# Optimization experiments

Hardware: AMD Instinct MI355X
Metric: run time of the kernel (lower is better)

The kernel has to match this reference:

```python
import jax, jax.numpy as jnp
import numpy as np

N, D0, D1, D2 = 8192, 512, 256, 64


def setup_inputs() -> dict:
    key = jax.random.key(0)
    k1, k2, k3, k4 = jax.random.split(key, 4)
    xi = jax.random.normal(k1, (N, D0), dtype=jnp.float32)
    # graph filter ~ row-normalized adjacency: nonnegative, entries O(1/N)
    filter_matrix = jax.random.uniform(k2, (N, N), dtype=jnp.float32) * (2.0 / N)
    b1 = np.sqrt(6.0 / (D0 + D1))
    b2 = np.sqrt(6.0 / (D1 + D2))
    w1 = jax.random.uniform(k3, (D0, D1), dtype=jnp.float32, minval=-b1, maxval=b1)
    w2 = jax.random.uniform(k4, (D1, D2), dtype=jnp.float32, minval=-b2, maxval=b2)
    return {"xi": xi, "filter_matrix": filter_matrix, "w1": w1, "w2": w2}


def reference(xi, filter_matrix, w1, w2):
    # two GCN layers: F @ (X @ W)
    h = jax.nn.relu(filter_matrix @ (xi @ w1))          # [N, D1]
    emb = filter_matrix @ (h @ w2)                       # [N, D2]
    # pairwise squared Euclidean distances between rows of emb -> [N, N]
    sq = jnp.sum(emb * emb, axis=1)                      # [N]
    dists = jnp.maximum(sq[:, None] + sq[None, :] - 2.0 * (emb @ emb.T), 0.0)
    recons_w = jax.nn.softmax(-dists, axis=1)            # row softmax of negative distances
    return emb, recons_w + 1e-10
```

## Files before the change

### kernel.cpp

```cpp
#include <hip/hip_runtime.h>

typedef short s16x8 __attribute__((ext_vector_type(8)));
typedef float f32x4 __attribute__((ext_vector_type(4)));
typedef unsigned int u32;

#define DEV static __device__ __forceinline__

DEV unsigned short f2bf(float x){
  u32 u = __builtin_bit_cast(u32, x);
  return (unsigned short)((u + 0x7FFFu + ((u >> 16) & 1u)) >> 16);
}
DEV float bf2f(unsigned short h){ u32 u = ((u32)h) << 16; return __builtin_bit_cast(float, u); }
DEV u32 pack2(float a, float b){ return (u32)f2bf(a) | ((u32)f2bf(b) << 16); }

DEV void gld16(const void* g, void* l){
  __builtin_amdgcn_global_load_lds((const __attribute__((address_space(1))) u32*)g,
                                   (__attribute__((address_space(3))) u32*)l, 16, 0, 0);
}

template<int N> DEV void vmwait(){
  static_assert(N>=0 && N<=8, "vmcnt range");
  if constexpr (N==0) asm volatile("s_waitcnt vmcnt(0)" ::: "memory");
  else if constexpr (N==1) asm volatile("s_waitcnt vmcnt(1)" ::: "memory");
  else if constexpr (N==2) asm volatile("s_waitcnt vmcnt(2)" ::: "memory");
  else if constexpr (N==3) asm volatile("s_waitcnt vmcnt(3)" ::: "memory");
  else if constexpr (N==4) asm volatile("s_waitcnt vmcnt(4)" ::: "memory");
  else if constexpr (N==5) asm volatile("s_waitcnt vmcnt(5)" ::: "memory");
  else if constexpr (N==6) asm volatile("s_waitcnt vmcnt(6)" ::: "memory");
  else if constexpr (N==7) asm volatile("s_waitcnt vmcnt(7)" ::: "memory");
  else                     asm volatile("s_waitcnt vmcnt(8)" ::: "memory");
}
DEV void pipebar(){
  __builtin_amdgcn_sched_barrier(0);
  __builtin_amdgcn_s_barrier();
  __builtin_amdgcn_sched_barrier(0);
}

__global__ void k_cvt(const float* __restrict__ src, unsigned short* __restrict__ dst, long n4){
  long i = (long)blockIdx.x*256 + threadIdx.x;
  long stride = (long)gridDim.x*256;
  for (; i < n4; i += stride){
    float4 v = ((const float4*)src)[i];
    int2 p; p.x = (int)pack2(v.x, v.y); p.y = (int)pack2(v.z, v.w);
    ((int2*)dst)[i] = p;
  }
}

__global__ void k_transpose_bf16(const float* __restrict__ src,
                                 unsigned short* __restrict__ dst, int R, int C){
  int idx = blockIdx.x * 256 + threadIdx.x;
  if (idx >= R * C) return;
  int r = idx / C, c = idx % C;
  dst[(size_t)c * R + r] = f2bf(src[idx]);
}

__global__ void k_relu_bf16(const float* __restrict__ src, unsigned short* __restrict__ dst, int n4){
  int idx = blockIdx.x*256 + threadIdx.x;
  if (idx >= n4) return;
  float4 v = ((const float4*)src)[idx];
  int2 p;
  p.x = (int)pack2(fmaxf(v.x,0.f), fmaxf(v.y,0.f));
  p.y = (int)pack2(fmaxf(v.z,0.f), fmaxf(v.w,0.f));
  ((int2*)dst)[idx] = p;
}

template<int ROWS,int BK,int THREADS>
DEV void stage_lds(const unsigned short* __restrict__ src, int row0, int ld,
                   int kk, char* lds, int tid){
  constexpr int SLOTS = BK/8, SLM = SLOTS-1, RPC = 64/SLOTS;
  constexpr int NCH = ROWS*BK*2/1024;
  constexpr int NW = THREADS/64, NI = NCH/NW;
  static_assert(NI*NW==NCH, "chunk exact");
  const int lane = tid & 63, wid = tid >> 6;
  #pragma unroll
  for (int i=0;i<NI;i++){
    int c = i*NW + wid;
    int r = c*RPC + lane/SLOTS;
    int s = lane & SLM;
    int ks = s ^ (r & SLM);
    gld16(src + (size_t)(row0+r)*ld + kk + ks*8, lds + c*1024);
  }
}

template<int BM,int BN,int BK,int WR,int WC,bool ATOMIC>
__global__ __launch_bounds__(WR*WC*64)
void k_gemm(const unsigned short* __restrict__ A, const unsigned short* __restrict__ B,
            void* __restrict__ Cp, int lda, int ldb, int ldc, int kchunk)
{
  constexpr int THREADS = WR*WC*64;
  constexpr int ROWB = BK*2, SLM = BK/8 - 1;
  constexpr int TBYTES = (BM+BN)*ROWB;
  constexpr int WM = BM/WR, WN = BN/WC;
  constexpr int FM = WM/16, FN = WN/16, KS = BK/32;
  constexpr int LA = BM*BK*2/1024/(THREADS/64);
  constexpr int LB = BN*BK*2/1024/(THREADS/64);
  constexpr int L  = LA + LB;

  __shared__ char smem[3*TBYTES];

  const int tid = threadIdx.x, lane = tid & 63;
  const int wid = tid >> 6, wrr = wid / WC, wcc = wid % WC;
  const int m0 = blockIdx.y * BM, n0 = blockIdx.x * BN;
  const int kbeg = blockIdx.z * kchunk, nk = kchunk / BK;

  f32x4 acc[FM][FN];
  f32x4 z4 = {0.f,0.f,0.f,0.f};
  #pragma unroll
  for (int m=0;m<FM;m++)
    #pragma unroll
    for (int n=0;n<FN;n++) acc[m][n] = z4;

  auto stage = [&](int kk, char* b){
    stage_lds<BM,BK,THREADS>(A, m0, lda, kk, b, tid);
    stage_lds<BN,BK,THREADS>(B, n0, ldb, kk, b + BM*ROWB, tid);
  };
  auto compute = [&](const char* b){
    const char* bA = b;
    const char* bB = b + BM*ROWB;
    #pragma unroll
    for (int ks=0;ks<KS;ks++){
      s16x8 av[FM], bv[FN];
      #pragma unroll
      for (int m=0;m<FM;m++){
        int r = wrr*WM + m*16 + (lane&15);
        int s = (ks*4 + (lane>>4)) ^ (r & SLM);
        av[m] = *(const s16x8*)(bA + r*ROWB + s*16);
      }
      #pragma unroll
      for (int n=0;n<FN;n++){
        int r = wcc*WN + n*16 + (lane&15);
        int s = (ks*4 + (lane>>4)) ^ (r & SLM);
        bv[n] = *(const s16x8*)(bB + r*ROWB + s*16);
      }
      #pragma unroll
      for (int m=0;m<FM;m++)
        #pragma unroll
        for (int n=0;n<FN;n++)
          acc[m][n] = __builtin_amdgcn_mfma_f32_16x16x32_bf16(av[m], bv[n], acc[m][n], 0, 0, 0);
    }
  };

  char* bc = smem;
  char* b1 = smem + TBYTES;
  char* b2 = smem + 2*TBYTES;

  stage(kbeg, bc);
  stage(kbeg + BK, b1);

  for (int t=0; t<nk; t++){
    if (t+1 < nk) vmwait<L>();
    else          vmwait<0>();
    pipebar();
    if (t+2 < nk) stage(kbeg + (t+2)*BK, b2);
    compute(bc);
    pipebar();
    char* tmp = bc; bc = b1; b1 = b2; b2 = tmp;
  }

  if constexpr (ATOMIC) {
    float* Cf = (float*)Cp;
    #pragma unroll
    for (int m=0;m<FM;m++)
      #pragma unroll
      for (int n=0;n<FN;n++)
        #pragma unroll
        for (int r=0;r<4;r++){
          int row = m0 + wrr*WM + m*16 + (lane>>4)*4 + r;
          int col = n0 + wcc*WN + n*16 + (lane&15);
          atomicAdd(Cf + (size_t)row*ldc + col, acc[m][n][r]);
        }
  } else {
    unsigned short* Ch = (unsigned short*)Cp;
    #pragma unroll
    for (int m=0;m<FM;m++)
      #pragma unroll
      for (int n=0;n<FN;n++)
        #pragma unroll
        for (int r=0;r<4;r++){
          int row = m0 + wrr*WM + m*16 + (lane>>4)*4 + r;
          int col = n0 + wcc*WN + n*16 + (lane&15);
          Ch[(size_t)row*ldc + col] = f2bf(acc[m][n][r]);
        }
  }
}

__global__ void k_emb_fin(const float* __restrict__ acc, float* __restrict__ emb_out,
                          unsigned short* __restrict__ embb, float* __restrict__ sq){
  int idx = blockIdx.x*256 + threadIdx.x;
  float v = acc[idx];
  emb_out[idx] = v;
  unsigned short ub = f2bf(v);
  embb[idx] = ub;
  float x = bf2f(ub);
  float s = x*x;
  #pragma unroll
  for (int off=32; off>0; off>>=1) s += __shfl_xor(s, off, 64);
  if ((threadIdx.x & 63)==0) sq[idx>>6] = s;
}

template<int PASS>
__global__ __launch_bounds__(256)
void k_dist(const unsigned short* __restrict__ embb, const float* __restrict__ sq,
            float* __restrict__ S, float* __restrict__ out)
{
  constexpr int ROWB = 128, SLM = 7;
  __shared__ char smem[2*128*128];
  char* bufA = smem;
  char* bufB = smem + 128*ROWB;
  const int tid=threadIdx.x, lane=tid&63, wid=tid>>6;
  const int wrr = wid>>1, wcc = wid&1;
  const int i0 = blockIdx.y*128, j0 = blockIdx.x*128;

  #pragma unroll
  for (int i=0;i<4;i++){
    int u = tid + i*256;
    int r = u>>3, c = u&7;
    int byte = r*ROWB + ((c^(r&SLM))*16);
    *(int4*)(bufA+byte) = *(const int4*)(embb + (size_t)(i0+r)*64 + c*8);
    *(int4*)(bufB+byte) = *(const int4*)(embb + (size_t)(j0+r)*64 + c*8);
  }
  __syncthreads();

  f32x4 acc[4][4];
  f32x4 z4 = {0.f,0.f,0.f,0.f};
  #pragma unroll
  for (int m=0;m<4;m++)
    #pragma unroll
    for (int n=0;n<4;n++) acc[m][n]=z4;

  #pragma unroll
  for (int ks=0;ks<2;ks++){
    s16x8 av[4], bv[4];
    #pragma unroll
    for (int m=0;m<4;m++){
      int r = wrr*64 + m*16 + (lane&15);
      int slot = (ks*4 + (lane>>4)) ^ (r&SLM);
      av[m] = *(const s16x8*)(bufA + r*ROWB + slot*16);
    }
    #pragma unroll
    for (int n=0;n<4;n++){
      int r = wcc*64 + n*16 + (lane&15);
      int slot = (ks*4 + (lane>>4)) ^ (r&SLM);
      bv[n] = *(const s16x8*)(bufB + r*ROWB + slot*16);
    }
    #pragma unroll
    for (int m=0;m<4;m++)
      #pragma unroll
      for (int n=0;n<4;n++)
        acc[m][n] = __builtin_amdgcn_mfma_f32_16x16x32_bf16(av[m], bv[n], acc[m][n], 0, 0, 0);
  }

  float sqj[4];
  #pragma unroll
  for (int n=0;n<4;n++) sqj[n] = sq[j0 + wcc*64 + n*16 + (lane&15)];

  #pragma unroll
  for (int m=0;m<4;m++){
    #pragma unroll
    for (int r=0;r<4;r++){
      int row = i0 + wrr*64 + m*16 + (lane>>4)*4 + r;
      float sqi = sq[row];
      if constexpr (PASS==1){
        float v = 0.f;
        #pragma unroll
        for (int n=0;n<4;n++){
          float d = fmaxf(sqi + sqj[n] - 2.f*acc[m][n][r], 0.f);
          v += __expf(-d);
        }
        #pragma unroll
        for (int off=1; off<16; off<<=1) v += __shfl_xor(v, off, 64);
        if ((lane&15)==0) atomicAdd(S+row, v);
      } else {
        float inv = 1.0f / S[row];
        #pragma unroll
        for (int n=0;n<4;n++){
          int col = j0 + wcc*64 + n*16 + (lane&15);
          float d = fmaxf(sqi + sqj[n] - 2.f*acc[m][n][r], 0.f);
          out[(size_t)row*8192 + col] = __expf(-d)*inv + 1e-10f;
        }
      }
    }
  }
}

extern "C" void kernel_launch(void* const* d_in, const int* in_sizes, int n_in,
                              void* d_out, int out_size, void* d_ws, size_t ws_size,
                              hipStream_t stream)
{
  const float* xi = (const float*)d_in[0];
  const float* F  = (const float*)d_in[1];
  const float* w1 = (const float*)d_in[2];
  const float* w2 = (const float*)d_in[3];
  float* out = (float*)d_out;
  float* emb_out = out;
  float* recons  = out + (size_t)8192*64;

  unsigned short* Fb = (unsigned short*)recons;

  char* ws = (char*)d_ws;
  size_t off = 0;
  auto alloc = [&](size_t bytes)->char*{ char* p = ws + off; off += (bytes + 255) & ~(size_t)255; return p; };
  unsigned short* w1t  = (unsigned short*)alloc((size_t)256*512*2);
  unsigned short* w2t  = (unsigned short*)alloc((size_t)64*256*2);
  unsigned short* xib  = (unsigned short*)alloc((size_t)8192*512*2);
  unsigned short* t1t  = (unsigned short*)alloc((size_t)256*8192*2);
  unsigned short* t2t  = (unsigned short*)alloc((size_t)64*8192*2);
  unsigned short* h    = (unsigned short*)alloc((size_t)8192*256*2);
  unsigned short* embb = (unsigned short*)alloc((size_t)8192*64*2);
  float* sq    = (float*)alloc((size_t)8192*4);
  char* zbase = ws + off;
  float* h_acc   = (float*)alloc((size_t)8192*256*4);
  float* emb_acc = (float*)alloc((size_t)8192*64*4);
  float* S       = (float*)alloc((size_t)8192*4);
  size_t zbytes = (size_t)((ws + off) - zbase);

  hipMemsetAsync(zbase, 0, zbytes, stream);

  k_cvt<<<dim3(2048),256,0,stream>>>(F,  Fb,  (long)8192*8192/4);
  k_cvt<<<dim3(2048),256,0,stream>>>(xi, xib, (long)8192*512/4);
  k_transpose_bf16<<<dim3((512*256+255)/256), 256, 0, stream>>>(w1, w1t, 512, 256);
  k_transpose_bf16<<<dim3((256*64+255)/256),  256, 0, stream>>>(w2, w2t, 256, 64);

  k_gemm<128,64,64,2,2,false><<<dim3(128,2,1),256,0,stream>>>(
      w1t, xib, t1t, 512, 512, 8192, 512);

  k_gemm<128,256,32,2,4,true><<<dim3(1,64,8),512,0,stream>>>(
      Fb, t1t, h_acc, 8192, 8192, 256, 1024);

  k_relu_bf16<<<dim3(8192*256/4/256),256,0,stream>>>(h_acc, h, 8192*256/4);

  k_gemm<64,64,64,2,2,false><<<dim3(128,1,1),256,0,stream>>>(
      w2t, h, t2t, 256, 256, 8192, 256);

  k_gemm<128,64,64,2,2,true><<<dim3(1,64,8),256,0,stream>>>(
      Fb, t2t, emb_acc, 8192, 8192, 64, 1024);

  k_emb_fin<<<dim3(8192*64/256),256,0,stream>>>(emb_acc, emb_out, embb, sq);

  k_dist<1><<<dim3(64,64),256,0,stream>>>(embb, sq, S, recons);
  k_dist<2><<<dim3(64,64),256,0,stream>>>(embb, sq, S, recons);
}
```

Before: 351.2 us.

## Fuse fp32-to-bf16 conversion and ReLU into GEMM operand loading

Removes the standalone conversion kernels for F and xi and the ReLU kernel. The GEMMs now load fp32 operands into registers, then convert them (applying ReLU where needed) and write them into swizzled LDS. The first F GEMM also writes the bf16 copy of F back to global memory for the second F GEMM, which saves one full fp32 pass over the 256MB matrix. It also merges the weight transposes into one prep kernel, changes the LDS swizzle for BK=32, and adds occupancy hints, at the cost of more register pressure and more complex vmcnt accounting.

```diff
diff --git a/kernel.cpp b/kernel.cpp
--- a/kernel.cpp
+++ b/kernel.cpp
@@ -19,7 +19,7 @@
 }
 
 template<int N> DEV void vmwait(){
-  static_assert(N>=0 && N<=8, "vmcnt range");
+  static_assert(N>=0 && N<=16, "vmcnt range");
   if constexpr (N==0) asm volatile("s_waitcnt vmcnt(0)" ::: "memory");
   else if constexpr (N==1) asm volatile("s_waitcnt vmcnt(1)" ::: "memory");
   else if constexpr (N==2) asm volatile("s_waitcnt vmcnt(2)" ::: "memory");
@@ -28,46 +28,32 @@
   else if constexpr (N==5) asm volatile("s_waitcnt vmcnt(5)" ::: "memory");
   else if constexpr (N==6) asm volatile("s_waitcnt vmcnt(6)" ::: "memory");
   else if constexpr (N==7) asm volatile("s_waitcnt vmcnt(7)" ::: "memory");
-  else                     asm volatile("s_waitcnt vmcnt(8)" ::: "memory");
+  else if constexpr (N==8) asm volatile("s_waitcnt vmcnt(8)" ::: "memory");
+  else if constexpr (N==9) asm volatile("s_waitcnt vmcnt(9)" ::: "memory");
+  else if constexpr (N==10) asm volatile("s_waitcnt vmcnt(10)" ::: "memory");
+  else if constexpr (N==11) asm volatile("s_waitcnt vmcnt(11)" ::: "memory");
+  else if constexpr (N==12) asm volatile("s_waitcnt vmcnt(12)" ::: "memory");
+  else                      asm volatile("s_waitcnt vmcnt(16)" ::: "memory");
 }
 DEV void pipebar(){
   __builtin_amdgcn_sched_barrier(0);
   __builtin_amdgcn_s_barrier();
   __builtin_amdgcn_sched_barrier(0);
 }
-
-__global__ void k_cvt(const float* __restrict__ src, unsigned short* __restrict__ dst, long n4){
-  long i = (long)blockIdx.x*256 + threadIdx.x;
-  long stride = (long)gridDim.x*256;
-  for (; i < n4; i += stride){
-    float4 v = ((const float4*)src)[i];
-    int2 p; p.x = (int)pack2(v.x, v.y); p.y = (int)pack2(v.z, v.w);
-    ((int2*)dst)[i] = p;
-  }
-}
-
-__global__ void k_transpose_bf16(const float* __restrict__ src,
-                                 unsigned short* __restrict__ dst, int R, int C){
-  int idx = blockIdx.x * 256 + threadIdx.x;
-  if (idx >= R * C) return;
-  int r = idx / C, c = idx % C;
-  dst[(size_t)c * R + r] = f2bf(src[idx]);
-}
-
-__global__ void k_relu_bf16(const float* __restrict__ src, unsigned short* __restrict__ dst, int n4){
+DEV void lgkm0(){ asm volatile("s_waitcnt lgkmcnt(0)" ::: "memory"); }
+
+__global__ void k_prep(const float* __restrict__ w1, const float* __restrict__ w2,
+                       unsigned short* __restrict__ w1t, unsigned short* __restrict__ w2t){
   int idx = blockIdx.x*256 + threadIdx.x;
-  if (idx >= n4) return;
-  float4 v = ((const float4*)src)[idx];
-  int2 p;
-  p.x = (int)pack2(fmaxf(v.x,0.f), fmaxf(v.y,0.f));
-  p.y = (int)pack2(fmaxf(v.z,0.f), fmaxf(v.w,0.f));
-  ((int2*)dst)[idx] = p;
+  if (idx < 512*256){ int r=idx/256, c=idx%256; w1t[(size_t)c*512 + r] = f2bf(w1[idx]); }
+  else { int j = idx - 512*256; if (j < 256*64){ int r=j/64, c=j%64; w2t[(size_t)c*256 + r] = f2bf(w2[j]); } }
 }
 
 template<int ROWS,int BK,int THREADS>
 DEV void stage_lds(const unsigned short* __restrict__ src, int row0, int ld,
                    int kk, char* lds, int tid){
   constexpr int SLOTS = BK/8, SLM = SLOTS-1, RPC = 64/SLOTS;
+  constexpr int RSH = (SLOTS==4) ? 1 : 0;
   constexpr int NCH = ROWS*BK*2/1024;
   constexpr int NW = THREADS/64, NI = NCH/NW;
   static_assert(NI*NW==NCH, "chunk exact");
@@ -77,24 +63,67 @@
     int c = i*NW + wid;
     int r = c*RPC + lane/SLOTS;
     int s = lane & SLM;
-    int ks = s ^ (r & SLM);
+    int ks = s ^ ((r>>RSH)&SLM);
     gld16(src + (size_t)(row0+r)*ld + kk + ks*8, lds + c*1024);
   }
 }
 
-template<int BM,int BN,int BK,int WR,int WC,bool ATOMIC>
-__global__ __launch_bounds__(WR*WC*64)
-void k_gemm(const unsigned short* __restrict__ A, const unsigned short* __restrict__ B,
-            void* __restrict__ Cp, int lda, int ldb, int ldc, int kchunk)
+template<int ROWS,int BK,int THREADS,int NC8>
+DEV void f32_load(const float* __restrict__ src, int row0, int ld, int kk,
+                  float4* regs, int tid){
+  constexpr int CPR = BK/8;
+  #pragma unroll
+  for (int i=0;i<NC8;i++){
+    int v = tid + i*THREADS;
+    int r = v/CPR, c = v%CPR;
+    const float* p = src + (size_t)(row0+r)*ld + kk + c*8;
+    regs[2*i]   = *(const float4*)p;
+    regs[2*i+1] = *(const float4*)(p+4);
+  }
+}
+template<int ROWS,int BK,int THREADS,int NC8,bool RELU,bool WB>
+DEV void f32_write(const float4* regs, char* lds, unsigned short* __restrict__ gdst,
+                   int row0, int gld_, int kk, int tid){
+  constexpr int CPR = BK/8, SLOTS = BK/8, SLM = SLOTS-1, ROWB = BK*2;
+  constexpr int RSH = (SLOTS==4) ? 1 : 0;
+  #pragma unroll
+  for (int i=0;i<NC8;i++){
+    int v = tid + i*THREADS;
+    int r = v/CPR, c = v%CPR;
+    float4 x = regs[2*i], y = regs[2*i+1];
+    if constexpr (RELU){
+      x.x=fmaxf(x.x,0.f); x.y=fmaxf(x.y,0.f); x.z=fmaxf(x.z,0.f); x.w=fmaxf(x.w,0.f);
+      y.x=fmaxf(y.x,0.f); y.y=fmaxf(y.y,0.f); y.z=fmaxf(y.z,0.f); y.w=fmaxf(y.w,0.f);
+    }
+    int4 p; p.x=(int)pack2(x.x,x.y); p.y=(int)pack2(x.z,x.w);
+            p.z=(int)pack2(y.x,y.y); p.w=(int)pack2(y.z,y.w);
+    int s = c ^ ((r>>RSH)&SLM);
+    *(int4*)(lds + r*ROWB + s*16) = p;
+    if constexpr (WB)
+      *(int4*)(gdst + (size_t)(row0+r)*gld_ + kk + c*8) = p;
+  }
+}
+
+template<int BM,int BN,int BK,int WR,int WC,bool AF32,bool BF32,bool ATOMIC,bool BRELU,bool AWB>
+__global__ __launch_bounds__(WR*WC*64, (WR*WC==8)?4:2)
+void k_gemm(const void* __restrict__ Ap, const void* __restrict__ Bp,
+            void* __restrict__ Cp, unsigned short* __restrict__ Awb,
+            int lda, int ldb, int ldc, int kchunk)
 {
   constexpr int THREADS = WR*WC*64;
-  constexpr int ROWB = BK*2, SLM = BK/8 - 1;
+  constexpr int ROWB = BK*2, SLOTS = BK/8, SLM = SLOTS-1;
+  constexpr int RSH = (SLOTS==4) ? 1 : 0;
   constexpr int TBYTES = (BM+BN)*ROWB;
   constexpr int WM = BM/WR, WN = BN/WC;
   constexpr int FM = WM/16, FN = WN/16, KS = BK/32;
-  constexpr int LA = BM*BK*2/1024/(THREADS/64);
-  constexpr int LB = BN*BK*2/1024/(THREADS/64);
-  constexpr int L  = LA + LB;
+  constexpr int NC8A = AF32 ? BM*BK/(8*THREADS) : 0;
+  constexpr int NC8B = BF32 ? BN*BK/(8*THREADS) : 0;
+  constexpr int LAb  = AF32 ? 0 : BM*ROWB/1024/(THREADS/64);
+  constexpr int LBb  = BF32 ? 0 : BN*ROWB/1024/(THREADS/64);
+  constexpr int L  = 2*NC8A + 2*NC8B + LAb + LBb;
+  constexpr int NS = AWB ? NC8A : 0;
+  constexpr int MA = AF32 ? 2*NC8A : 1;
+  constexpr int MB = BF32 ? 2*NC8B : 1;
 
   __shared__ char smem[3*TBYTES];
 
@@ -103,6 +132,11 @@
   const int m0 = blockIdx.y * BM, n0 = blockIdx.x * BN;
   const int kbeg = blockIdx.z * kchunk, nk = kchunk / BK;
 
+  const float* Af = (const float*)Ap;
+  const unsigned short* Ah = (const unsigned short*)Ap;
+  const float* Bf = (const float*)Bp;
+  const unsigned short* Bh = (const unsigned short*)Bp;
+
   f32x4 acc[FM][FN];
   f32x4 z4 = {0.f,0.f,0.f,0.f};
   #pragma unroll
@@ -110,26 +144,32 @@
     #pragma unroll
     for (int n=0;n<FN;n++) acc[m][n] = z4;
 
-  auto stage = [&](int kk, char* b){
-    stage_lds<BM,BK,THREADS>(A, m0, lda, kk, b, tid);
-    stage_lds<BN,BK,THREADS>(B, n0, ldb, kk, b + BM*ROWB, tid);
+  auto stage = [&](float4* ar, float4* br, int kk, char* buf){
+    if constexpr (AF32) f32_load<BM,BK,THREADS,NC8A>(Af, m0, lda, kk, ar, tid);
+    else                stage_lds<BM,BK,THREADS>(Ah, m0, lda, kk, buf, tid);
+    if constexpr (BF32) f32_load<BN,BK,THREADS,NC8B>(Bf, n0, ldb, kk, br, tid);
+    else                stage_lds<BN,BK,THREADS>(Bh, n0, ldb, kk, buf + BM*ROWB, tid);
   };
-  auto compute = [&](const char* b){
-    const char* bA = b;
-    const char* bB = b + BM*ROWB;
+  auto wrt = [&](const float4* ar, const float4* br, char* buf, int kk){
+    if constexpr (AF32) f32_write<BM,BK,THREADS,NC8A,false,AWB>(ar, buf, Awb, m0, lda, kk, tid);
+    if constexpr (BF32) f32_write<BN,BK,THREADS,NC8B,BRELU,false>(br, buf + BM*ROWB, (unsigned short*)0, n0, ldb, kk, tid);
+  };
+  auto compute = [&](const char* buf){
+    const char* bA = buf;
+    const char* bB = buf + BM*ROWB;
     #pragma unroll
     for (int ks=0;ks<KS;ks++){
       s16x8 av[FM], bv[FN];
       #pragma unroll
       for (int m=0;m<FM;m++){
         int r = wrr*WM + m*16 + (lane&15);
-        int s = (ks*4 + (lane>>4)) ^ (r & SLM);
+        int s = (ks*4 + (lane>>4)) ^ ((r>>RSH)&SLM);
         av[m] = *(const s16x8*)(bA + r*ROWB + s*16);
       }
       #pragma unroll
       for (int n=0;n<FN;n++){
         int r = wcc*WN + n*16 + (lane&15);
-        int s = (ks*4 + (lane>>4)) ^ (r & SLM);
+        int s = (ks*4 + (lane>>4)) ^ ((r>>RSH)&SLM);
         bv[n] = *(const s16x8*)(bB + r*ROWB + s*16);
       }
       #pragma unroll
@@ -141,20 +181,32 @@
   };
 
   char* bc = smem;
-  char* b1 = smem + TBYTES;
-  char* b2 = smem + 2*TBYTES;
-
-  stage(kbeg, bc);
-  stage(kbeg + BK, b1);
-
-  for (int t=0; t<nk; t++){
-    if (t+1 < nk) vmwait<L>();
-    else          vmwait<0>();
+  char* bn_ = smem + TBYTES;
+  char* bf_ = smem + 2*TBYTES;
+
+  float4 a0[MA], a1[MA], b0[MB], b1[MB];
+
+  stage(a0, b0, kbeg,      bc);
+  stage(a1, b1, kbeg + BK, bn_);
+
+  auto iterate = [&](int t, float4* ar, float4* br){
+    if (t == 0)            vmwait<L>();
+    else if (t >= nk-1)    vmwait<NS>();
+    else                   vmwait<L+NS>();
+    if constexpr (AF32 || BF32){
+      wrt(ar, br, bc, kbeg + t*BK);
+      lgkm0();
+    }
     pipebar();
-    if (t+2 < nk) stage(kbeg + (t+2)*BK, b2);
+    if (t+2 < nk) stage(ar, br, kbeg + (t+2)*BK, bf_);
     compute(bc);
     pipebar();
-    char* tmp = bc; bc = b1; b1 = b2; b2 = tmp;
+    char* tmp = bc; bc = bn_; bn_ = bf_; bf_ = tmp;
+  };
+
+  for (int t = 0; t < nk; t += 2){
+    iterate(t,   a0, b0);
+    iterate(t+1, a1, b1);
   }
 
   if constexpr (ATOMIC) {
@@ -302,10 +354,8 @@
   auto alloc = [&](size_t bytes)->char*{ char* p = ws + off; off += (bytes + 255) & ~(size_t)255; return p; };
   unsigned short* w1t  = (unsigned short*)alloc((size_t)256*512*2);
   unsigned short* w2t  = (unsigned short*)alloc((size_t)64*256*2);
-  unsigned short* xib  = (unsigned short*)alloc((size_t)8192*512*2);
   unsigned short* t1t  = (unsigned short*)alloc((size_t)256*8192*2);
   unsigned short* t2t  = (unsigned short*)alloc((size_t)64*8192*2);
-  unsigned short* h    = (unsigned short*)alloc((size_t)8192*256*2);
   unsigned short* embb = (unsigned short*)alloc((size_t)8192*64*2);
   float* sq    = (float*)alloc((size_t)8192*4);
   char* zbase = ws + off;
@@ -316,24 +366,19 @@
 
   hipMemsetAsync(zbase, 0, zbytes, stream);
 
-  k_cvt<<<dim3(2048),256,0,stream>>>(F,  Fb,  (long)8192*8192/4);
-  k_cvt<<<dim3(2048),256,0,stream>>>(xi, xib, (long)8192*512/4);
-  k_transpose_bf16<<<dim3((512*256+255)/256), 256, 0, stream>>>(w1, w1t, 512, 256);
-  k_transpose_bf16<<<dim3((256*64+255)/256),  256, 0, stream>>>(w2, w2t, 256, 64);
-
-  k_gemm<128,64,64,2,2,false><<<dim3(128,2,1),256,0,stream>>>(
-      w1t, xib, t1t, 512, 512, 8192, 512);
-
-  k_gemm<128,256,32,2,4,true><<<dim3(1,64,8),512,0,stream>>>(
-      Fb, t1t, h_acc, 8192, 8192, 256, 1024);
-
-  k_relu_bf16<<<dim3(8192*256/4/256),256,0,stream>>>(h_acc, h, 8192*256/4);
-
-  k_gemm<64,64,64,2,2,false><<<dim3(128,1,1),256,0,stream>>>(
-      w2t, h, t2t, 256, 256, 8192, 256);
-
-  k_gemm<128,64,64,2,2,true><<<dim3(1,64,8),256,0,stream>>>(
-      Fb, t2t, emb_acc, 8192, 8192, 64, 1024);
+  k_prep<<<dim3((512*256 + 256*64)/256), 256, 0, stream>>>(w1, w2, w1t, w2t);
+
+  k_gemm<128,64,64,2,2,false,true,false,false,false><<<dim3(128,2,1),256,0,stream>>>(
+      w1t, xi, t1t, nullptr, 512, 512, 8192, 512);
+
+  k_gemm<128,256,32,2,4,true,false,true,false,true><<<dim3(1,64,8),512,0,stream>>>(
+      F, t1t, h_acc, Fb, 8192, 8192, 256, 1024);
+
+  k_gemm<64,64,64,2,2,false,true,false,true,false><<<dim3(128,1,1),256,0,stream>>>(
+      w2t, h_acc, t2t, nullptr, 256, 256, 8192, 256);
+
+  k_gemm<128,64,64,2,2,false,false,true,false,false><<<dim3(1,64,8),256,0,stream>>>(
+      Fb, t2t, emb_acc, nullptr, 8192, 8192, 64, 1024);
 
   k_emb_fin<<<dim3(8192*64/256),256,0,stream>>>(emb_acc, emb_out, embb, sq);
 
```

New measurement: 375.4 us. +6.9%, slower.

## Replace split-K atomics with partial buffers and reduce, fix swizzle, merge prep kernels

Applied to the files above, without the earlier changes.

The split-K GEMMs now write plain per-slice partial buffers instead of doing fp32 atomicAdds, and separate reduce kernels sum the 8 slices (fused with ReLU and bf16 conversion for h). This removes atomic contention and the large memset. The LDS swizzle changes for BK=32 tiles to avoid bank conflicts, the weight transposes merge into one kernel, and a few launch shapes and occupancy hints change. In exchange the partial buffers add extra global memory traffic (8 slices of h and emb).

```diff
diff --git a/kernel.cpp b/kernel.cpp
--- a/kernel.cpp
+++ b/kernel.cpp
@@ -46,28 +46,18 @@
   }
 }
 
-__global__ void k_transpose_bf16(const float* __restrict__ src,
-                                 unsigned short* __restrict__ dst, int R, int C){
-  int idx = blockIdx.x * 256 + threadIdx.x;
-  if (idx >= R * C) return;
-  int r = idx / C, c = idx % C;
-  dst[(size_t)c * R + r] = f2bf(src[idx]);
-}
-
-__global__ void k_relu_bf16(const float* __restrict__ src, unsigned short* __restrict__ dst, int n4){
+__global__ void k_prep(const float* __restrict__ w1, const float* __restrict__ w2,
+                       unsigned short* __restrict__ w1t, unsigned short* __restrict__ w2t){
   int idx = blockIdx.x*256 + threadIdx.x;
-  if (idx >= n4) return;
-  float4 v = ((const float4*)src)[idx];
-  int2 p;
-  p.x = (int)pack2(fmaxf(v.x,0.f), fmaxf(v.y,0.f));
-  p.y = (int)pack2(fmaxf(v.z,0.f), fmaxf(v.w,0.f));
-  ((int2*)dst)[idx] = p;
+  if (idx < 512*256){ int r=idx/256, c=idx%256; w1t[(size_t)c*512 + r] = f2bf(w1[idx]); }
+  else { int j = idx - 512*256; if (j < 256*64){ int r=j/64, c=j%64; w2t[(size_t)c*256 + r] = f2bf(w2[j]); } }
 }
 
 template<int ROWS,int BK,int THREADS>
 DEV void stage_lds(const unsigned short* __restrict__ src, int row0, int ld,
                    int kk, char* lds, int tid){
   constexpr int SLOTS = BK/8, SLM = SLOTS-1, RPC = 64/SLOTS;
+  constexpr int RSH = (SLOTS==4) ? 1 : 0;
   constexpr int NCH = ROWS*BK*2/1024;
   constexpr int NW = THREADS/64, NI = NCH/NW;
   static_assert(NI*NW==NCH, "chunk exact");
@@ -77,23 +67,24 @@
     int c = i*NW + wid;
     int r = c*RPC + lane/SLOTS;
     int s = lane & SLM;
-    int ks = s ^ (r & SLM);
+    int ks = s ^ ((r>>RSH)&SLM);
     gld16(src + (size_t)(row0+r)*ld + kk + ks*8, lds + c*1024);
   }
 }
 
-template<int BM,int BN,int BK,int WR,int WC,bool ATOMIC>
-__global__ __launch_bounds__(WR*WC*64)
+template<int BM,int BN,int BK,int WR,int WC,bool PART>
+__global__ __launch_bounds__(WR*WC*64, (WR*WC>=8)?4:2)
 void k_gemm(const unsigned short* __restrict__ A, const unsigned short* __restrict__ B,
-            void* __restrict__ Cp, int lda, int ldb, int ldc, int kchunk)
+            void* __restrict__ Cp, int lda, int ldb, int ldc, int kchunk, long pstride)
 {
   constexpr int THREADS = WR*WC*64;
-  constexpr int ROWB = BK*2, SLM = BK/8 - 1;
+  constexpr int ROWB = BK*2, SLOTS = BK/8, SLM = SLOTS-1;
+  constexpr int RSH = (SLOTS==4) ? 1 : 0;
   constexpr int TBYTES = (BM+BN)*ROWB;
   constexpr int WM = BM/WR, WN = BN/WC;
   constexpr int FM = WM/16, FN = WN/16, KS = BK/32;
-  constexpr int LA = BM*BK*2/1024/(THREADS/64);
-  constexpr int LB = BN*BK*2/1024/(THREADS/64);
+  constexpr int LA = BM*ROWB/1024/(THREADS/64);
+  constexpr int LB = BN*ROWB/1024/(THREADS/64);
   constexpr int L  = LA + LB;
 
   __shared__ char smem[3*TBYTES];
@@ -110,26 +101,26 @@
     #pragma unroll
     for (int n=0;n<FN;n++) acc[m][n] = z4;
 
-  auto stage = [&](int kk, char* b){
-    stage_lds<BM,BK,THREADS>(A, m0, lda, kk, b, tid);
-    stage_lds<BN,BK,THREADS>(B, n0, ldb, kk, b + BM*ROWB, tid);
+  auto stage = [&](int kk, char* buf){
+    stage_lds<BM,BK,THREADS>(A, m0, lda, kk, buf, tid);
+    stage_lds<BN,BK,THREADS>(B, n0, ldb, kk, buf + BM*ROWB, tid);
   };
-  auto compute = [&](const char* b){
-    const char* bA = b;
-    const char* bB = b + BM*ROWB;
+  auto compute = [&](const char* buf){
+    const char* bA = buf;
+    const char* bB = buf + BM*ROWB;
     #pragma unroll
     for (int ks=0;ks<KS;ks++){
       s16x8 av[FM], bv[FN];
       #pragma unroll
       for (int m=0;m<FM;m++){
         int r = wrr*WM + m*16 + (lane&15);
-        int s = (ks*4 + (lane>>4)) ^ (r & SLM);
+        int s = (ks*4 + (lane>>4)) ^ ((r>>RSH)&SLM);
         av[m] = *(const s16x8*)(bA + r*ROWB + s*16);
       }
       #pragma unroll
       for (int n=0;n<FN;n++){
         int r = wcc*WN + n*16 + (lane&15);
-        int s = (ks*4 + (lane>>4)) ^ (r & SLM);
+        int s = (ks*4 + (lane>>4)) ^ ((r>>RSH)&SLM);
         bv[n] = *(const s16x8*)(bB + r*ROWB + s*16);
       }
       #pragma unroll
@@ -140,25 +131,25 @@
     }
   };
 
-  char* bc = smem;
-  char* b1 = smem + TBYTES;
-  char* b2 = smem + 2*TBYTES;
+  char* bc  = smem;
+  char* bn_ = smem + TBYTES;
+  char* bf_ = smem + 2*TBYTES;
 
   stage(kbeg, bc);
-  stage(kbeg + BK, b1);
+  stage(kbeg + BK, bn_);
 
   for (int t=0; t<nk; t++){
     if (t+1 < nk) vmwait<L>();
     else          vmwait<0>();
     pipebar();
-    if (t+2 < nk) stage(kbeg + (t+2)*BK, b2);
+    if (t+2 < nk) stage(kbeg + (t+2)*BK, bf_);
     compute(bc);
     pipebar();
-    char* tmp = bc; bc = b1; b1 = b2; b2 = tmp;
-  }
-
-  if constexpr (ATOMIC) {
-    float* Cf = (float*)Cp;
+    char* tmp = bc; bc = bn_; bn_ = bf_; bf_ = tmp;
+  }
+
+  if constexpr (PART) {
+    float* Cf = (float*)Cp + (size_t)blockIdx.z * pstride;
     #pragma unroll
     for (int m=0;m<FM;m++)
       #pragma unroll
@@ -167,7 +158,7 @@
         for (int r=0;r<4;r++){
           int row = m0 + wrr*WM + m*16 + (lane>>4)*4 + r;
           int col = n0 + wcc*WN + n*16 + (lane&15);
-          atomicAdd(Cf + (size_t)row*ldc + col, acc[m][n][r]);
+          Cf[(size_t)row*ldc + col] = acc[m][n][r];
         }
   } else {
     unsigned short* Ch = (unsigned short*)Cp;
@@ -184,10 +175,28 @@
   }
 }
 
-__global__ void k_emb_fin(const float* __restrict__ acc, float* __restrict__ emb_out,
+__global__ void k_hred(const float* __restrict__ hp, unsigned short* __restrict__ h){
+  const long N = (long)8192*256/4;
+  long i = (long)blockIdx.x*256 + threadIdx.x;
+  if (i >= N) return;
+  float4 s = ((const float4*)hp)[i];
+  #pragma unroll
+  for (int z=1; z<8; z++){
+    float4 v = ((const float4*)(hp + (size_t)z*8192*256))[i];
+    s.x+=v.x; s.y+=v.y; s.z+=v.z; s.w+=v.w;
+  }
+  int2 p;
+  p.x = (int)pack2(fmaxf(s.x,0.f), fmaxf(s.y,0.f));
+  p.y = (int)pack2(fmaxf(s.z,0.f), fmaxf(s.w,0.f));
+  ((int2*)h)[i] = p;
+}
+
+__global__ void k_emb_fin(const float* __restrict__ ep, float* __restrict__ emb_out,
                           unsigned short* __restrict__ embb, float* __restrict__ sq){
   int idx = blockIdx.x*256 + threadIdx.x;
-  float v = acc[idx];
+  float v = 0.f;
+  #pragma unroll
+  for (int z=0; z<8; z++) v += ep[(size_t)z*8192*64 + idx];
   emb_out[idx] = v;
   unsigned short ub = f2bf(v);
   embb[idx] = ub;
@@ -307,35 +316,32 @@
   unsigned short* t2t  = (unsigned short*)alloc((size_t)64*8192*2);
   unsigned short* h    = (unsigned short*)alloc((size_t)8192*256*2);
   unsigned short* embb = (unsigned short*)alloc((size_t)8192*64*2);
-  float* sq    = (float*)alloc((size_t)8192*4);
-  char* zbase = ws + off;
-  float* h_acc   = (float*)alloc((size_t)8192*256*4);
-  float* emb_acc = (float*)alloc((size_t)8192*64*4);
-  float* S       = (float*)alloc((size_t)8192*4);
-  size_t zbytes = (size_t)((ws + off) - zbase);
-
-  hipMemsetAsync(zbase, 0, zbytes, stream);
-
+  float* sq     = (float*)alloc((size_t)8192*4);
+  float* h_part = (float*)alloc((size_t)8*8192*256*4);
+  float* e_part = (float*)alloc((size_t)8*8192*64*4);
+  float* S      = (float*)alloc((size_t)8192*4);
+
+  hipMemsetAsync(S, 0, (size_t)8192*4, stream);
+
+  k_prep<<<dim3((512*256 + 256*64)/256), 256, 0, stream>>>(w1, w2, w1t, w2t);
   k_cvt<<<dim3(2048),256,0,stream>>>(F,  Fb,  (long)8192*8192/4);
-  k_cvt<<<dim3(2048),256,0,stream>>>(xi, xib, (long)8192*512/4);
-  k_transpose_bf16<<<dim3((512*256+255)/256), 256, 0, stream>>>(w1, w1t, 512, 256);
-  k_transpose_bf16<<<dim3((256*64+255)/256),  256, 0, stream>>>(w2, w2t, 256, 64);
+  k_cvt<<<dim3(256), 256,0,stream>>>(xi, xib, (long)8192*512/4);
 
   k_gemm<128,64,64,2,2,false><<<dim3(128,2,1),256,0,stream>>>(
-      w1t, xib, t1t, 512, 512, 8192, 512);
+      w1t, xib, t1t, 512, 512, 8192, 512, 0);
 
   k_gemm<128,256,32,2,4,true><<<dim3(1,64,8),512,0,stream>>>(
-      Fb, t1t, h_acc, 8192, 8192, 256, 1024);
-
-  k_relu_bf16<<<dim3(8192*256/4/256),256,0,stream>>>(h_acc, h, 8192*256/4);
-
-  k_gemm<64,64,64,2,2,false><<<dim3(128,1,1),256,0,stream>>>(
-      w2t, h, t2t, 256, 256, 8192, 256);
+      Fb, t1t, h_part, 8192, 8192, 256, 1024, (long)8192*256);
+
+  k_hred<<<dim3(2048),256,0,stream>>>(h_part, h);
+
+  k_gemm<64,32,64,2,2,false><<<dim3(256,1,1),256,0,stream>>>(
+      w2t, h, t2t, 256, 256, 8192, 256, 0);
 
   k_gemm<128,64,64,2,2,true><<<dim3(1,64,8),256,0,stream>>>(
-      Fb, t2t, emb_acc, 8192, 8192, 64, 1024);
-
-  k_emb_fin<<<dim3(8192*64/256),256,0,stream>>>(emb_acc, emb_out, embb, sq);
+      Fb, t2t, e_part, 8192, 8192, 64, 1024, (long)8192*64);
+
+  k_emb_fin<<<dim3(8192*64/256),256,0,stream>>>(e_part, emb_out, embb, sq);
 
   k_dist<1><<<dim3(64,64),256,0,stream>>>(embb, sq, S, recons);
   k_dist<2><<<dim3(64,64),256,0,stream>>>(embb, sq, S, recons);
```

Measured after the change: 348.1 us. About the same (-0.9%).
